# Kernel optimization log

Measured on AMD Instinct MI355X. Metric: run time of the kernel, lower is better.

## Reference

```python
import jax, jax.numpy as jnp
import numpy as np

B = 32768
NPG = 15            # nodes per graph (5 segments * 3 nodes)
NSEG = 5
FEAT = 8
HID = 64
BIAS_SP = float(np.log(np.exp(1.0) - 1.0))  # biased_softplus_1.0 bias
SCALE_LB = 1e-4


def _edge_template():
    eg = []
    for s in range(NSEG):
        t = 3 * s
        eg += [(t, t + 1), (t + 1, t), (t, t + 2), (t + 2, t)]
    for s in range(NSEG - 1):
        eg += [(3 * s, 3 * s + 3), (3 * s + 3, 3 * s)]
    return np.asarray(eg, dtype=np.int64)  # [28, 2]


def setup_inputs() -> dict:
    key = jax.random.key(0)
    ks = jax.random.split(key, 16)
    N = B * NPG
    x = jax.random.normal(ks[0], (N, FEAT), dtype=jnp.float32)
    tmpl = _edge_template()
    offs = (np.arange(B, dtype=np.int64) * NPG)[:, None]          # [B,1]
    src = (tmpl[:, 0][None, :] + offs).ravel()
    dst = (tmpl[:, 1][None, :] + offs).ravel()
    edge_index = jnp.asarray(np.stack([src, dst]), dtype=jnp.int32)  # [2,E]
    sd = 0.05
    params = dict(
        Wt=jax.random.normal(ks[1], (FEAT, HID), jnp.float32) * sd,
        bt=jax.random.normal(ks[2], (HID,), jnp.float32) * sd,
        Wl=jax.random.normal(ks[3], (4, HID), jnp.float32) * sd,
        bl=jax.random.normal(ks[4], (HID,), jnp.float32) * sd,
        gc_Wroot=jax.random.normal(ks[5], (3, HID, HID), jnp.float32) * sd,
        gc_Wrel=jax.random.normal(ks[6], (3, HID, HID), jnp.float32) * sd,
        gc_b=jax.random.normal(ks[7], (3, HID), jnp.float32) * sd,
        leg_W=jax.random.normal(ks[8], (10, HID, 4), jnp.float32) * sd,
        leg_b=jax.random.normal(ks[9], (10, 4), jnp.float32) * sd,
        torso_W=jax.random.normal(ks[10], (4, HID, 4), jnp.float32) * sd,
        torso_b=jax.random.normal(ks[11], (4, 4), jnp.float32) * sd,
    )
    return dict(x=x, edge_index=edge_index, batch_size=B, **params)


def reference(x, edge_index, batch_size, Wt, bt, Wl, bl,
              gc_Wroot, gc_Wrel, gc_b, leg_W, leg_b, torso_W, torso_b):
    N = x.shape[0]
    npg = N // batch_size              # 15
    nseg = npg // 3                    # 5
    pos = jnp.arange(N) % npg
    is_torso = (pos % 3) == 0          # nodes 0,3,6,... within each graph

    # Per-type input encoders + tanh, merged by mask (original scatters into h)
    h_t = jnp.tanh(x @ Wt + bt)
    h_l = jnp.tanh(x[:, :4] @ Wl + bl)
    h = jnp.where(is_torso[:, None], h_t, h_l)        # [N, 64]

    src, dst = edge_index[0], edge_index[1]
    for i in range(3):
        agg = jax.ops.segment_sum(h[src], dst, num_segments=N)
        h = jnp.tanh(agg @ gc_Wrel[i] + gc_b[i] + h @ gc_Wroot[i])

    hp = h.reshape(batch_size, npg, HID)              # [B, 15, 64]

    leg_pos = jnp.array([p for p in range(1, npg) if p % 3 != 0])   # 10 legs
    torso_pos = jnp.array([3 * s for s in range(1, nseg)])          # 4 torsos

    leg_out = jnp.einsum('bnd,ndk->bnk', hp[:, leg_pos], leg_W) + leg_b      # [B,10,4]
    torso_out = jnp.einsum('bnd,ndk->bnk', hp[:, torso_pos], torso_W) + torso_b  # [B,4,4]

    # Blocks are emitted in node-position order 1..14 within each graph
    blocks = jnp.zeros((batch_size, npg - 1, 4), dtype=h.dtype)
    blocks = blocks.at[:, leg_pos - 1].set(leg_out)
    blocks = blocks.at[:, torso_pos - 1].set(torso_out)
    out = blocks.reshape(batch_size, 2 * (npg - 1), 2)               # [B,28,2]

    loc = out[..., 0]
    scale = jnp.maximum(jax.nn.softplus(out[..., 1] + BIAS_SP), SCALE_LB)
    return loc, scale
```

## Files before the change

### kernel.cpp

```cpp
#include <hip/hip_runtime.h>

#define NB 32768
#define GPB 4
#define THREADS 256
#define BIAS_SP 0.5413248546129181f

typedef __attribute__((ext_vector_type(8))) short bf16x8;
typedef __attribute__((ext_vector_type(4))) float f32x4;
typedef __attribute__((ext_vector_type(4))) unsigned int u32x4;

static __device__ __forceinline__ unsigned f2bfu(float f) {
    union { float f; unsigned u; } v; v.f = f;
    return (v.u + 0x8000u) >> 16;
}
static __device__ __forceinline__ float bf2f(unsigned short s) {
    union { unsigned u; float f; } v; v.u = ((unsigned)s) << 16;
    return v.f;
}
static __device__ __forceinline__ float lof(unsigned u) {
    union { unsigned u; float f; } v; v.u = u << 16; return v.f;
}
static __device__ __forceinline__ float hif(unsigned u) {
    union { unsigned u; float f; } v; v.u = u & 0xFFFF0000u; return v.f;
}
static __device__ __forceinline__ float fast_tanh(float xx) {
    float e = __expf(2.0f * xx);
    return 1.0f - 2.0f * __builtin_amdgcn_rcpf(e + 1.0f);
}

__global__ void setup_kernel(const float* __restrict__ Wroot, const float* __restrict__ Wrel,
                             const float* __restrict__ legW, const float* __restrict__ torW,
                             unsigned* __restrict__ wsw) {
    const int t = blockIdx.x * 256 + threadIdx.x;
    if (t < 3072) {
        const int i = t >> 10, rem = t & 1023, s = rem >> 8, tt = rem & 255;
        const int lane = tt & 63, ctl = tt >> 6;
        const int bcol = (ctl << 4) + (lane & 15);
        const int kb = ((s & 1) << 5) + ((lane >> 4) << 3);
        const float* M = ((s < 2) ? Wroot : Wrel) + i * 4096 + kb * 64 + bcol;
        u32x4 d;
        #pragma unroll
        for (int dd = 0; dd < 4; ++dd)
            d[dd] = f2bfu(M[(2 * dd) * 64]) | (f2bfu(M[(2 * dd + 1) * 64]) << 16);
        *(u32x4*)(wsw + t * 4) = d;
    } else if (t < 3520) {
        const int t2 = t - 3072, item = t2 >> 3, k8 = t2 & 7;
        const int p = (item >> 2) + 1, j = item & 3;
        const int p3 = (p * 11) >> 5;
        const int pm3 = p - p3 * 3;
        const float* src;
        if (pm3 == 0) src = torW + (p3 - 1) * 256 + j;
        else          src = legW + (2 * p3 + pm3 - 1) * 256 + j;
        u32x4 d;
        #pragma unroll
        for (int dd = 0; dd < 4; ++dd) {
            const int k = (k8 << 3) + 2 * dd;
            d[dd] = f2bfu(src[k * 4]) | (f2bfu(src[(k + 1) * 4]) << 16);
        }
        *(u32x4*)(wsw + 12288 + t2 * 4) = d;
    }
}

#define RDH(r) bf2f(*(const unsigned short*)(smem + wbase + (r) * 256 + (colb ^ (((r) & 7) << 4))))
#define WRA(r, v) *(unsigned short*)(smem + wbase + (r) * 256 + 128 + (colb ^ (((r) & 7) << 4))) = (unsigned short)f2bfu(v)
#define AGG() do { \
    float s0  = RDH(1)  + RDH(2)  + RDH(3); \
    float s3  = RDH(4)  + RDH(5)  + RDH(0) + RDH(6); \
    float s6  = RDH(7)  + RDH(8)  + RDH(3) + RDH(9); \
    float s9  = RDH(10) + RDH(11) + RDH(6) + RDH(12); \
    float s12 = RDH(13) + RDH(14) + RDH(9); \
    WRA(0, s0); WRA(3, s3); WRA(6, s6); WRA(9, s9); WRA(12, s12); \
} while (0)

__global__ __launch_bounds__(THREADS, 4) void leg_main(
    const float* __restrict__ x,
    const float* __restrict__ Wt, const float* __restrict__ bt,
    const float* __restrict__ Wl, const float* __restrict__ bl,
    const float* __restrict__ gcb,
    const float* __restrict__ legB, const float* __restrict__ torB,
    const unsigned* __restrict__ wsw,
    float* __restrict__ out)
{
    __shared__ __align__(16) unsigned char smem[GPB * 4096];
    const int tid  = threadIdx.x;
    const int lane = tid & 63;
    const int ct   = tid >> 6;
    const int g0   = blockIdx.x * GPB;
    const int wbase = ct * 4096;

    bf16x8 bfr[3][4];
    #pragma unroll
    for (int i = 0; i < 3; ++i)
        #pragma unroll
        for (int s = 0; s < 4; ++s)
            bfr[i][s] = *(const bf16x8*)(wsw + ((i * 4 + s) * 256 + tid) * 4);
    const int bcol = (ct << 4) + (lane & 15);
    const float cb0 = gcb[bcol], cb1 = gcb[64 + bcol], cb2 = gcb[128 + bcol];

    const int colb = ((lane >> 3) << 4) + ((lane & 7) << 1);
    const int row = lane & 15, kg = lane >> 4;
    const int row3 = (row * 11) >> 5;
    const int tors = row3 * 3;
    const int isT  = (row == tors);
    const int rowR = isT ? row : tors;
    const int voffA0 = row * 256 + (((kg ^ row) & 7) << 4);
    const int voffA2 = rowR * 256 + (((kg ^ rowR) & 7) << 4) + (isT ? 128 : 0);
    int voffC[4];
    #pragma unroll
    for (int r = 0; r < 4; ++r) {
        const int rr = (kg << 2) + r;
        voffC[r] = rr * 256 + (((((ct << 1) + ((lane >> 3) & 1)) ^ rr) & 7) << 4) + ((lane & 7) << 1);
    }

    float ewt[8], ewl[4];
    #pragma unroll
    for (int k = 0; k < 8; ++k) ewt[k] = Wt[(k << 6) + lane];
    #pragma unroll
    for (int k = 0; k < 4; ++k) ewl[k] = Wl[(k << 6) + lane];
    const float ebt = bt[lane], ebl = bl[lane];

    const float4* xg = (const float4*)(x + (size_t)(g0 + ct) * 120);
    #pragma unroll
    for (int p = 0; p < 15; ++p) {
        const float4 a0 = xg[p * 2];
        float acc;
        if (p % 3 == 0) {
            const float4 a1 = xg[p * 2 + 1];
            acc = ebt + a0.x * ewt[0] + a0.y * ewt[1] + a0.z * ewt[2] + a0.w * ewt[3]
                      + a1.x * ewt[4] + a1.y * ewt[5] + a1.z * ewt[6] + a1.w * ewt[7];
        } else {
            acc = ebl + a0.x * ewl[0] + a0.y * ewl[1] + a0.z * ewl[2] + a0.w * ewl[3];
        }
        *(unsigned short*)(smem + wbase + p * 256 + (colb ^ ((p & 7) << 4))) =
            (unsigned short)f2bfu(fast_tanh(acc));
    }
    *(unsigned short*)(smem + wbase + 15 * 256 + (colb ^ 0x70)) = 0;
    *(unsigned short*)(smem + wbase + 15 * 256 + 128 + (colb ^ 0x70)) = 0;

    AGG();
    __syncthreads();

    #pragma unroll
    for (int it = 0; it < 3; ++it) {
        const float cbi = (it == 0) ? cb0 : (it == 1) ? cb1 : cb2;
        f32x4 acc[GPB];
        #pragma unroll
        for (int g = 0; g < GPB; ++g) {
            const unsigned char* sg = smem + g * 4096;
            const bf16x8 a0 = *(const bf16x8*)(sg + voffA0);
            const bf16x8 a1 = *(const bf16x8*)(sg + (voffA0 ^ 0x40));
            const bf16x8 a2 = *(const bf16x8*)(sg + voffA2);
            const bf16x8 a3 = *(const bf16x8*)(sg + (voffA2 ^ 0x40));
            f32x4 c = { cbi, cbi, cbi, cbi };
            c = __builtin_amdgcn_mfma_f32_16x16x32_bf16(a0, bfr[it][0], c, 0, 0, 0);
            c = __builtin_amdgcn_mfma_f32_16x16x32_bf16(a1, bfr[it][1], c, 0, 0, 0);
            c = __builtin_amdgcn_mfma_f32_16x16x32_bf16(a2, bfr[it][2], c, 0, 0, 0);
            c = __builtin_amdgcn_mfma_f32_16x16x32_bf16(a3, bfr[it][3], c, 0, 0, 0);
            acc[g] = c;
        }
        __syncthreads();
        #pragma unroll
        for (int g = 0; g < GPB; ++g)
            #pragma unroll
            for (int r = 0; r < 4; ++r)
                *(unsigned short*)(smem + g * 4096 + voffC[r]) =
                    (unsigned short)f2bfu(fast_tanh(acc[g][r]));
        __syncthreads();
        if (it < 2) { AGG(); __syncthreads(); }
    }

    if (lane < 56) {
        const int p = (lane >> 2) + 1, j = lane & 3;
        const int p3 = (p * 11) >> 5;
        const int pm3 = p - p3 * 3;
        float bias;
        if (pm3 == 0) bias = torB[((p3 - 1) << 2) + j];
        else          bias = legB[(((p3 << 1) + pm3 - 1) << 2) + j];
        const unsigned* wp = wsw + 12288 + (lane << 5);
        const unsigned char* hb = smem + wbase + p * 256;
        const int ps = (p & 7) << 4;
        float acc = 0.f;
        #pragma unroll
        for (int k8 = 0; k8 < 8; ++k8) {
            const u32x4 hv = *(const u32x4*)(hb + (ps ^ (k8 << 4)));
            const u32x4 wv = *(const u32x4*)(wp + (k8 << 2));
            #pragma unroll
            for (int dd = 0; dd < 4; ++dd) {
                acc = __builtin_fmaf(lof(hv[dd]), lof(wv[dd]), acc);
                acc = __builtin_fmaf(hif(hv[dd]), hif(wv[dd]), acc);
            }
        }
        acc += bias;
        const int mloc = ((p - 1) << 1) + (j >> 1);
        const size_t ob = (size_t)(g0 + ct) * 28 + mloc;
        if ((j & 1) == 0) {
            out[ob] = acc;
        } else {
            const float z = acc + BIAS_SP;
            const float sp = (z > 15.f) ? z : __logf(1.f + __expf(z));
            out[(size_t)NB * 28 + ob] = fmaxf(sp, 1e-4f);
        }
    }
}

extern "C" void kernel_launch(void* const* d_in, const int* in_sizes, int n_in,
                              void* d_out, int out_size, void* d_ws, size_t ws_size,
                              hipStream_t stream) {
    (void)in_sizes; (void)n_in; (void)out_size; (void)ws_size;
    const float* x     = (const float*)d_in[0];
    const float* Wt    = (const float*)d_in[3];
    const float* bt    = (const float*)d_in[4];
    const float* Wl    = (const float*)d_in[5];
    const float* bl    = (const float*)d_in[6];
    const float* Wroot = (const float*)d_in[7];
    const float* Wrel  = (const float*)d_in[8];
    const float* gcb   = (const float*)d_in[9];
    const float* legW  = (const float*)d_in[10];
    const float* legB  = (const float*)d_in[11];
    const float* torW  = (const float*)d_in[12];
    const float* torB  = (const float*)d_in[13];
    unsigned* wsw = (unsigned*)d_ws;
    setup_kernel<<<14, 256, 0, stream>>>(Wroot, Wrel, legW, torW, wsw);
    leg_main<<<NB / GPB, 256, 0, stream>>>(x, Wt, bt, Wl, bl, gcb, legB, torB, wsw,
                                           (float*)d_out);
}
```

Before: 82.96 us.

## Process eight graphs per block with packed bf16x2 aggregation and per-layer weight loads

Doubles graphs per block to 8, so each wave encodes and decodes two graphs and the MFMA B-fragments are reused across twice as many graphs. The neighbour aggregation now reads and writes 32-bit pairs of bf16 values with half a wave per graph instead of 16-bit scalars. GraphConv weights are loaded per layer rather than all held in registers, which lowers register pressure so the occupancy hint can rise to 5. In exchange shared memory per block doubles to 32 KB, there are fewer blocks, and each layer adds global weight loads.

```diff
diff --git a/kernel.cpp b/kernel.cpp
--- a/kernel.cpp
+++ b/kernel.cpp
@@ -1,7 +1,7 @@
 #include <hip/hip_runtime.h>
 
 #define NB 32768
-#define GPB 4
+#define GPB 8
 #define THREADS 256
 #define BIAS_SP 0.5413248546129181f
 
@@ -13,9 +13,9 @@
     union { float f; unsigned u; } v; v.f = f;
     return (v.u + 0x8000u) >> 16;
 }
-static __device__ __forceinline__ float bf2f(unsigned short s) {
-    union { unsigned u; float f; } v; v.u = ((unsigned)s) << 16;
-    return v.f;
+static __device__ __forceinline__ unsigned f2bfu_hi(float f) {
+    union { float f; unsigned u; } v; v.f = f;
+    return (v.u + 0x8000u) & 0xFFFF0000u;
 }
 static __device__ __forceinline__ float lof(unsigned u) {
     union { unsigned u; float f; } v; v.u = u << 16; return v.f;
@@ -61,18 +61,7 @@
     }
 }
 
-#define RDH(r) bf2f(*(const unsigned short*)(smem + wbase + (r) * 256 + (colb ^ (((r) & 7) << 4))))
-#define WRA(r, v) *(unsigned short*)(smem + wbase + (r) * 256 + 128 + (colb ^ (((r) & 7) << 4))) = (unsigned short)f2bfu(v)
-#define AGG() do { \
-    float s0  = RDH(1)  + RDH(2)  + RDH(3); \
-    float s3  = RDH(4)  + RDH(5)  + RDH(0) + RDH(6); \
-    float s6  = RDH(7)  + RDH(8)  + RDH(3) + RDH(9); \
-    float s9  = RDH(10) + RDH(11) + RDH(6) + RDH(12); \
-    float s12 = RDH(13) + RDH(14) + RDH(9); \
-    WRA(0, s0); WRA(3, s3); WRA(6, s6); WRA(9, s9); WRA(12, s12); \
-} while (0)
-
-__global__ __launch_bounds__(THREADS, 4) void leg_main(
+__global__ __launch_bounds__(THREADS, 5) void leg_main(
     const float* __restrict__ x,
     const float* __restrict__ Wt, const float* __restrict__ bt,
     const float* __restrict__ Wl, const float* __restrict__ bl,
@@ -86,14 +75,7 @@
     const int lane = tid & 63;
     const int ct   = tid >> 6;
     const int g0   = blockIdx.x * GPB;
-    const int wbase = ct * 4096;
-
-    bf16x8 bfr[3][4];
-    #pragma unroll
-    for (int i = 0; i < 3; ++i)
-        #pragma unroll
-        for (int s = 0; s < 4; ++s)
-            bfr[i][s] = *(const bf16x8*)(wsw + ((i * 4 + s) * 256 + tid) * 4);
+
     const int bcol = (ct << 4) + (lane & 15);
     const float cb0 = gcb[bcol], cb1 = gcb[64 + bcol], cb2 = gcb[128 + bcol];
 
@@ -112,6 +94,23 @@
         voffC[r] = rr * 256 + (((((ct << 1) + ((lane >> 3) & 1)) ^ rr) & 7) << 4) + ((lane & 7) << 1);
     }
 
+    const int half = lane >> 5;
+    const int c2   = lane & 31;
+    unsigned char* gbase = smem + ((ct << 1) + half) * 4096;
+    const int aoff = (c2 & 3) << 2;
+#define RD32(r)  (*(const unsigned*)(gbase + (r) * 256 + (((((c2) >> 2) ^ (r)) & 7) << 4) + aoff))
+#define WR32(r, flo, fhi) *(unsigned*)(gbase + (r) * 256 + 128 + (((((c2) >> 2) ^ (r)) & 7) << 4) + aoff) = (f2bfu(flo) | f2bfu_hi(fhi))
+#define AGG() do { \
+    unsigned u[15]; \
+    _Pragma("unroll") for (int r = 0; r < 15; ++r) u[r] = RD32(r); \
+    float l3 = lof(u[3]), h3 = hif(u[3]), l6 = lof(u[6]), h6 = hif(u[6]), l9 = lof(u[9]), h9 = hif(u[9]); \
+    WR32(0,  lof(u[1]) + lof(u[2]) + l3,              hif(u[1]) + hif(u[2]) + h3); \
+    WR32(3,  lof(u[4]) + lof(u[5]) + lof(u[0]) + l6,  hif(u[4]) + hif(u[5]) + hif(u[0]) + h6); \
+    WR32(6,  lof(u[7]) + lof(u[8]) + l3 + l9,         hif(u[7]) + hif(u[8]) + h3 + h9); \
+    WR32(9,  lof(u[10]) + lof(u[11]) + l6 + lof(u[12]), hif(u[10]) + hif(u[11]) + h6 + hif(u[12])); \
+    WR32(12, lof(u[13]) + lof(u[14]) + l9,            hif(u[13]) + hif(u[14]) + h9); \
+} while (0)
+
     float ewt[8], ewl[4];
     #pragma unroll
     for (int k = 0; k < 8; ++k) ewt[k] = Wt[(k << 6) + lane];
@@ -119,29 +118,38 @@
     for (int k = 0; k < 4; ++k) ewl[k] = Wl[(k << 6) + lane];
     const float ebt = bt[lane], ebl = bl[lane];
 
-    const float4* xg = (const float4*)(x + (size_t)(g0 + ct) * 120);
-    #pragma unroll
-    for (int p = 0; p < 15; ++p) {
-        const float4 a0 = xg[p * 2];
-        float acc;
-        if (p % 3 == 0) {
-            const float4 a1 = xg[p * 2 + 1];
-            acc = ebt + a0.x * ewt[0] + a0.y * ewt[1] + a0.z * ewt[2] + a0.w * ewt[3]
-                      + a1.x * ewt[4] + a1.y * ewt[5] + a1.z * ewt[6] + a1.w * ewt[7];
-        } else {
-            acc = ebl + a0.x * ewl[0] + a0.y * ewl[1] + a0.z * ewl[2] + a0.w * ewl[3];
-        }
-        *(unsigned short*)(smem + wbase + p * 256 + (colb ^ ((p & 7) << 4))) =
-            (unsigned short)f2bfu(fast_tanh(acc));
-    }
-    *(unsigned short*)(smem + wbase + 15 * 256 + (colb ^ 0x70)) = 0;
-    *(unsigned short*)(smem + wbase + 15 * 256 + 128 + (colb ^ 0x70)) = 0;
-
+    #pragma unroll
+    for (int gs = 0; gs < 2; ++gs) {
+        const int g = (ct << 1) + gs;
+        const float4* xg = (const float4*)(x + (size_t)(g0 + g) * 120);
+        unsigned char* sb = smem + g * 4096;
+        #pragma unroll
+        for (int p = 0; p < 15; ++p) {
+            const float4 a0 = xg[p * 2];
+            float acc;
+            if (p % 3 == 0) {
+                const float4 a1 = xg[p * 2 + 1];
+                acc = ebt + a0.x * ewt[0] + a0.y * ewt[1] + a0.z * ewt[2] + a0.w * ewt[3]
+                          + a1.x * ewt[4] + a1.y * ewt[5] + a1.z * ewt[6] + a1.w * ewt[7];
+            } else {
+                acc = ebl + a0.x * ewl[0] + a0.y * ewl[1] + a0.z * ewl[2] + a0.w * ewl[3];
+            }
+            *(unsigned short*)(sb + p * 256 + (colb ^ ((p & 7) << 4))) =
+                (unsigned short)f2bfu(fast_tanh(acc));
+        }
+        *(unsigned short*)(sb + 15 * 256 + (colb ^ 0x70)) = 0;
+        *(unsigned short*)(sb + 15 * 256 + 128 + (colb ^ 0x70)) = 0;
+    }
+    __syncthreads();
     AGG();
     __syncthreads();
 
     #pragma unroll
     for (int it = 0; it < 3; ++it) {
+        bf16x8 bfr[4];
+        #pragma unroll
+        for (int s = 0; s < 4; ++s)
+            bfr[s] = *(const bf16x8*)(wsw + ((it * 4 + s) * 256 + tid) * 4);
         const float cbi = (it == 0) ? cb0 : (it == 1) ? cb1 : cb2;
         f32x4 acc[GPB];
         #pragma unroll
@@ -152,10 +160,10 @@
             const bf16x8 a2 = *(const bf16x8*)(sg + voffA2);
             const bf16x8 a3 = *(const bf16x8*)(sg + (voffA2 ^ 0x40));
             f32x4 c = { cbi, cbi, cbi, cbi };
-            c = __builtin_amdgcn_mfma_f32_16x16x32_bf16(a0, bfr[it][0], c, 0, 0, 0);
-            c = __builtin_amdgcn_mfma_f32_16x16x32_bf16(a1, bfr[it][1], c, 0, 0, 0);
-            c = __builtin_amdgcn_mfma_f32_16x16x32_bf16(a2, bfr[it][2], c, 0, 0, 0);
-            c = __builtin_amdgcn_mfma_f32_16x16x32_bf16(a3, bfr[it][3], c, 0, 0, 0);
+            c = __builtin_amdgcn_mfma_f32_16x16x32_bf16(a0, bfr[0], c, 0, 0, 0);
+            c = __builtin_amdgcn_mfma_f32_16x16x32_bf16(a1, bfr[1], c, 0, 0, 0);
+            c = __builtin_amdgcn_mfma_f32_16x16x32_bf16(a2, bfr[2], c, 0, 0, 0);
+            c = __builtin_amdgcn_mfma_f32_16x16x32_bf16(a3, bfr[3], c, 0, 0, 0);
             acc[g] = c;
         }
         __syncthreads();
@@ -177,28 +185,32 @@
         if (pm3 == 0) bias = torB[((p3 - 1) << 2) + j];
         else          bias = legB[(((p3 << 1) + pm3 - 1) << 2) + j];
         const unsigned* wp = wsw + 12288 + (lane << 5);
-        const unsigned char* hb = smem + wbase + p * 256;
         const int ps = (p & 7) << 4;
-        float acc = 0.f;
-        #pragma unroll
-        for (int k8 = 0; k8 < 8; ++k8) {
-            const u32x4 hv = *(const u32x4*)(hb + (ps ^ (k8 << 4)));
-            const u32x4 wv = *(const u32x4*)(wp + (k8 << 2));
+        #pragma unroll
+        for (int gs = 0; gs < 2; ++gs) {
+            const int g = (ct << 1) + gs;
+            const unsigned char* hb = smem + g * 4096 + p * 256;
+            float acc = 0.f;
             #pragma unroll
-            for (int dd = 0; dd < 4; ++dd) {
-                acc = __builtin_fmaf(lof(hv[dd]), lof(wv[dd]), acc);
-                acc = __builtin_fmaf(hif(hv[dd]), hif(wv[dd]), acc);
+            for (int k8 = 0; k8 < 8; ++k8) {
+                const u32x4 hv = *(const u32x4*)(hb + (ps ^ (k8 << 4)));
+                const u32x4 wv = *(const u32x4*)(wp + (k8 << 2));
+                #pragma unroll
+                for (int dd = 0; dd < 4; ++dd) {
+                    acc = __builtin_fmaf(lof(hv[dd]), lof(wv[dd]), acc);
+                    acc = __builtin_fmaf(hif(hv[dd]), hif(wv[dd]), acc);
+                }
             }
-        }
-        acc += bias;
-        const int mloc = ((p - 1) << 1) + (j >> 1);
-        const size_t ob = (size_t)(g0 + ct) * 28 + mloc;
-        if ((j & 1) == 0) {
-            out[ob] = acc;
-        } else {
-            const float z = acc + BIAS_SP;
-            const float sp = (z > 15.f) ? z : __logf(1.f + __expf(z));
-            out[(size_t)NB * 28 + ob] = fmaxf(sp, 1e-4f);
+            acc += bias;
+            const int mloc = ((p - 1) << 1) + (j >> 1);
+            const size_t ob = (size_t)(g0 + g) * 28 + mloc;
+            if ((j & 1) == 0) {
+                out[ob] = acc;
+            } else {
+                const float z = acc + BIAS_SP;
+                const float sp = (z > 15.f) ? z : __logf(1.f + __expf(z));
+                out[(size_t)NB * 28 + ob] = fmaxf(sp, 1e-4f);
+            }
         }
     }
 }
```

After: 79.03 us. -4.7%, faster.
